# Performance work log

Hardware: AMD Instinct MI355X
Metric: run time of the kernel (lower is better)

Reference implementation:

```python
import jax, jax.numpy as jnp
import numpy as np

B, S, D, UNITS = 8, 2048, 512, 512

def setup_inputs() -> dict:
    key = jax.random.key(0)
    k1, k2, k3, k4 = jax.random.split(key, 4)
    scale = 1.0 / np.sqrt(D)
    return {
        "x": jax.random.normal(k1, (B, S, D), dtype=jnp.float32),
        "Wq": jax.random.normal(k2, (D, UNITS), dtype=jnp.float32) * scale,
        "Wk": jax.random.normal(k3, (D, UNITS), dtype=jnp.float32) * scale,
        "Wv": jax.random.normal(k4, (D, UNITS), dtype=jnp.float32) * scale,
    }

def reference(x, Wq, Wk, Wv):
    # Q, K, V: [B, S, units]
    Q = jnp.einsum('bsd,du->bsu', x, Wq)
    Km = jnp.einsum('bsd,du->bsu', x, Wk)
    V = jnp.einsum('bsd,du->bsu', x, Wv)
    d_k = jnp.asarray(Wq.shape[-1], dtype=x.dtype)
    # scores: [B, S, S]
    scores = jnp.einsum('bqu,bku->bqk', Q, Km) / jnp.sqrt(d_k)
    attn = jax.nn.softmax(scores, axis=-1)
    return jnp.einsum('bqk,bku->bqu', attn, V)
```

## Files before the change

### kernel.cpp

```cpp
#include <hip/hip_runtime.h>

typedef __attribute__((ext_vector_type(8))) __bf16 bf16x8;
typedef __attribute__((ext_vector_type(4))) float f32x4;
typedef unsigned short u16;
typedef unsigned int u32;

#define VMCNT(n) asm volatile("s_waitcnt vmcnt(" #n ")" ::: "memory")

__device__ __forceinline__ u16 f2bf(float f) {
  union { float f; u32 u; } v; v.f = f;
  u32 r = v.u + 0x7FFFu + ((v.u >> 16) & 1u);
  return (u16)(r >> 16);
}
__device__ __forceinline__ float fexp2(float x) {
  float r; asm("v_exp_f32 %0, %1" : "=v"(r) : "v"(x)); return r;
}

__global__ __launch_bounds__(256) void cast_x_kernel(const float* __restrict__ x,
                                                     u16* __restrict__ xb, int n4) {
  int i = blockIdx.x * 256 + threadIdx.x;
  if (i >= n4) return;
  float4 v = reinterpret_cast<const float4*>(x)[i];
  ushort4 o;
  o.x = f2bf(v.x); o.y = f2bf(v.y); o.z = f2bf(v.z); o.w = f2bf(v.w);
  reinterpret_cast<ushort4*>(xb)[i] = o;
}

__global__ __launch_bounds__(1024) void transpose_w_kernel(const float* __restrict__ Wq,
                                                           const float* __restrict__ Wk,
                                                           const float* __restrict__ Wv,
                                                           u16* __restrict__ Wt) {
  const float* src = blockIdx.z == 0 ? Wq : (blockIdx.z == 1 ? Wk : Wv);
  u16* dst = Wt + (size_t)blockIdx.z * 512 * 512;
  __shared__ float tile[32][33];
  int u0 = blockIdx.x * 32, d0 = blockIdx.y * 32;
  tile[threadIdx.y][threadIdx.x] = src[(d0 + threadIdx.y) * 512 + u0 + threadIdx.x];
  __syncthreads();
  dst[(u0 + threadIdx.y) * 512 + d0 + threadIdx.x] = f2bf(tile[threadIdx.x][threadIdx.y]);
}

__global__ __launch_bounds__(256) void qkv_kernel(const u16* __restrict__ Xb,
                                                  const u16* __restrict__ Wt3,
                                                  u16* __restrict__ Q, u16* __restrict__ K,
                                                  u16* __restrict__ Vt) {
  __shared__ u16 As[3][128 * 32], Bs[3][128 * 32];
  const int bm = blockIdx.y * 128;
  const int bn = blockIdx.x * 128;
  const int z = blockIdx.z;
  const u16* A = Xb + (size_t)bm * 512;
  const u16* Bt = Wt3 + (size_t)z * 512 * 512 + (size_t)bn * 512;

  const int t = threadIdx.x;
  const int lane = t & 63;
  const int w = t >> 6;
  const int wr = w >> 1, wc = w & 1;
  const int la = lane & 15;
  const int q = lane >> 4;
  f32x4 acc[4][4] = {};

  auto stage = [&](int buf, int kt) {
    const int k0 = kt * 32;
#pragma unroll
    for (int it = 0; it < 2; ++it) {
      int c = it * 256 + t, row = c >> 2;
      int col = ((c & 3) ^ ((row >> 1) & 3)) << 3;
      __builtin_amdgcn_global_load_lds(
          (const __attribute__((address_space(1))) void*)(A + (size_t)row * 512 + k0 + col),
          (__attribute__((address_space(3))) void*)(&As[buf][c * 8]), 16, 0, 0);
    }
#pragma unroll
    for (int it = 0; it < 2; ++it) {
      int c = it * 256 + t, row = c >> 2;
      int col = ((c & 3) ^ ((row >> 1) & 3)) << 3;
      __builtin_amdgcn_global_load_lds(
          (const __attribute__((address_space(1))) void*)(Bt + (size_t)row * 512 + k0 + col),
          (__attribute__((address_space(3))) void*)(&Bs[buf][c * 8]), 16, 0, 0);
    }
  };

  auto body = [&](int buf) {
    bf16x8 a[4], b[4];
#pragma unroll
    for (int i = 0; i < 4; ++i) {
      int row = wr * 64 + i * 16 + la;
      a[i] = *reinterpret_cast<const bf16x8*>(&As[buf][row * 32 + ((q ^ ((row >> 1) & 3)) << 3)]);
    }
#pragma unroll
    for (int j = 0; j < 4; ++j) {
      int row = wc * 64 + j * 16 + la;
      b[j] = *reinterpret_cast<const bf16x8*>(&Bs[buf][row * 32 + ((q ^ ((row >> 1) & 3)) << 3)]);
    }
    __builtin_amdgcn_s_setprio(1);
#pragma unroll
    for (int i = 0; i < 4; ++i)
#pragma unroll
      for (int j = 0; j < 4; ++j)
        acc[i][j] = __builtin_amdgcn_mfma_f32_16x16x32_bf16(a[i], b[j], acc[i][j], 0, 0, 0);
    __builtin_amdgcn_s_setprio(0);
  };

  stage(0, 0); stage(1, 1);
  int cb = 0, sb = 2;
  for (int kt = 0; kt < 14; ++kt) {
    VMCNT(4);
    __builtin_amdgcn_s_barrier();
    stage(sb, kt + 2);
    body(cb);
    cb = (cb == 2) ? 0 : cb + 1;
    sb = (sb == 2) ? 0 : sb + 1;
  }
  VMCNT(4); __builtin_amdgcn_s_barrier(); body(2);
  VMCNT(0); __builtin_amdgcn_s_barrier(); body(0);

  const int r0 = q * 4, cn = lane & 15;
  if (z < 2) {
    u16* out = (z == 0) ? Q : K;
#pragma unroll
    for (int i = 0; i < 4; ++i)
#pragma unroll
      for (int j = 0; j < 4; ++j)
#pragma unroll
        for (int r = 0; r < 4; ++r) {
          int m = bm + 64 * wr + 16 * i + r0 + r;
          int n = bn + 64 * wc + 16 * j + cn;
          out[(size_t)m * 512 + n] = f2bf(acc[i][j][r]);
        }
  } else {
#pragma unroll
    for (int i = 0; i < 4; ++i)
#pragma unroll
      for (int j = 0; j < 4; ++j)
#pragma unroll
        for (int r = 0; r < 4; ++r) {
          int m = bm + 64 * wr + 16 * i + r0 + r;
          int u = bn + 64 * wc + 16 * j + cn;
          int b = m >> 11, s = m & 2047;
          Vt[((size_t)b * 512 + u) * 2048 + s] = f2bf(acc[i][j][r]);
        }
  }
}

__global__ __launch_bounds__(512) void scores8_kernel(const u16* __restrict__ Q,
                                                      const u16* __restrict__ K,
                                                      u16* __restrict__ S) {
  __shared__ u16 ring[4][2][256 * 32];
  const int bb = blockIdx.x;
  const int bm = blockIdx.y * 256;
  const int bn = blockIdx.z * 256;
  const u16* Aq = Q + (size_t)(bb * 2048 + bm) * 512;
  const u16* Bk = K + (size_t)(bb * 2048 + bn) * 512;

  const int t = threadIdx.x;
  const int lane = t & 63;
  const int wid = t >> 6;
  const int wm = wid >> 2, wn = wid & 3;
  const int la = lane & 15;
  const int q = lane >> 4;

  f32x4 acc[8][4] = {};

  auto stage = [&](int kt) {
    const int r = kt & 3;
    const int koff = kt * 32;
#pragma unroll
    for (int half = 0; half < 2; ++half) {
      int c = half * 512 + t;
      int row = c >> 2;
      int col = ((c & 3) ^ ((row >> 1) & 3)) << 3;
      __builtin_amdgcn_global_load_lds(
          (const __attribute__((address_space(1))) void*)(Aq + (size_t)row * 512 + koff + col),
          (__attribute__((address_space(3))) void*)(&ring[r][0][c * 8]), 16, 0, 0);
      __builtin_amdgcn_global_load_lds(
          (const __attribute__((address_space(1))) void*)(Bk + (size_t)row * 512 + koff + col),
          (__attribute__((address_space(3))) void*)(&ring[r][1][c * 8]), 16, 0, 0);
    }
  };

  auto body = [&](int kt) {
    const int r = kt & 3;
    const u16* At = ring[r][0];
    const u16* Bt = ring[r][1];
    bf16x8 bfr[4], afr[8];
#pragma unroll
    for (int j = 0; j < 4; ++j) {
      int row = wn * 64 + j * 16 + la;
      bfr[j] = *reinterpret_cast<const bf16x8*>(Bt + row * 32 + ((q ^ ((row >> 1) & 3)) << 3));
    }
#pragma unroll
    for (int i = 0; i < 8; ++i) {
      int row = wm * 128 + i * 16 + la;
      afr[i] = *reinterpret_cast<const bf16x8*>(At + row * 32 + ((q ^ ((row >> 1) & 3)) << 3));
    }
    __builtin_amdgcn_s_setprio(1);
#pragma unroll
    for (int i = 0; i < 8; ++i)
#pragma unroll
      for (int j = 0; j < 4; ++j)
        acc[i][j] = __builtin_amdgcn_mfma_f32_16x16x32_bf16(afr[i], bfr[j], acc[i][j], 0, 0, 0);
    __builtin_amdgcn_s_setprio(0);
  };

  stage(0); stage(1); stage(2);
  for (int kt = 0; kt < 13; ++kt) {
    VMCNT(8);
    __builtin_amdgcn_s_barrier();
    stage(kt + 3);
    body(kt);
  }
  VMCNT(8); __builtin_amdgcn_s_barrier(); body(13);
  VMCNT(4); __builtin_amdgcn_s_barrier(); body(14);
  VMCNT(0); __builtin_amdgcn_s_barrier(); body(15);

  u16* C = S + (size_t)bb * 2048 * 2048;
  const float scale = 0.06375872127f;
  const int r0h = q * 4;
#pragma unroll
  for (int i = 0; i < 8; ++i)
#pragma unroll
    for (int j = 0; j < 4; ++j)
#pragma unroll
      for (int r = 0; r < 4; ++r) {
        int m = bm + wm * 128 + i * 16 + r0h + r;
        int n = bn + wn * 64 + j * 16 + la;
        C[(size_t)m * 2048 + n] = f2bf(fexp2(acc[i][j][r] * scale));
      }
}

__global__ __launch_bounds__(256) void pv_kernel(const u16* __restrict__ S,
                                                 const u16* __restrict__ Vt,
                                                 float* __restrict__ out) {
  __shared__ u16 As[4][128 * 32], Bs[4][128 * 32];
  __shared__ float larr[128];
  const int id = blockIdx.x;
  const int b = id & 7;
  const int local = id >> 3;
  const int bn = (local & 3) * 128;
  const int bm = (local >> 2) * 128;

  const u16* A = S + (size_t)(b * 2048 + bm) * 2048;
  const u16* Bt = Vt + ((size_t)b * 512 + bn) * 2048;

  const int t = threadIdx.x;
  const int lane = t & 63;
  const int w = t >> 6;
  const int wr = w >> 1, wc = w & 1;
  const int la = lane & 15;
  const int q = lane >> 4;
  f32x4 acc[4][4] = {};
  float lacc[4] = {0.f, 0.f, 0.f, 0.f};

  auto stage = [&](int kt) {
    const int buf = kt & 3;
    const int k0 = kt * 32;
#pragma unroll
    for (int it = 0; it < 2; ++it) {
      int c = it * 256 + t, row = c >> 2;
      int col = ((c & 3) ^ ((row >> 1) & 3)) << 3;
      __builtin_amdgcn_global_load_lds(
          (const __attribute__((address_space(1))) void*)(A + (size_t)row * 2048 + k0 + col),
          (__attribute__((address_space(3))) void*)(&As[buf][c * 8]), 16, 0, 0);
    }
#pragma unroll
    for (int it = 0; it < 2; ++it) {
      int c = it * 256 + t, row = c >> 2;
      int col = ((c & 3) ^ ((row >> 1) & 3)) << 3;
      __builtin_amdgcn_global_load_lds(
          (const __attribute__((address_space(1))) void*)(Bt + (size_t)row * 2048 + k0 + col),
          (__attribute__((address_space(3))) void*)(&Bs[buf][c * 8]), 16, 0, 0);
    }
  };

  auto body = [&](int kt) {
    const int buf = kt & 3;
    bf16x8 a[4], bb[4];
#pragma unroll
    for (int i = 0; i < 4; ++i) {
      int row = wr * 64 + i * 16 + la;
      a[i] = *reinterpret_cast<const bf16x8*>(&As[buf][row * 32 + ((q ^ ((row >> 1) & 3)) << 3)]);
    }
    if (wc == 0) {
#pragma unroll
      for (int i = 0; i < 4; ++i) {
        float ls = 0.f;
#pragma unroll
        for (int e = 0; e < 8; ++e) ls += (float)a[i][e];
        lacc[i] += ls;
      }
    }
#pragma unroll
    for (int j = 0; j < 4; ++j) {
      int row = wc * 64 + j * 16 + la;
      bb[j] = *reinterpret_cast<const bf16x8*>(&Bs[buf][row * 32 + ((q ^ ((row >> 1) & 3)) << 3)]);
    }
    __builtin_amdgcn_s_setprio(1);
#pragma unroll
    for (int i = 0; i < 4; ++i)
#pragma unroll
      for (int j = 0; j < 4; ++j)
        acc[i][j] = __builtin_amdgcn_mfma_f32_16x16x32_bf16(a[i], bb[j], acc[i][j], 0, 0, 0);
    __builtin_amdgcn_s_setprio(0);
  };

  stage(0); stage(1); stage(2);
  for (int kt = 0; kt < 61; ++kt) {
    VMCNT(8);
    __builtin_amdgcn_s_barrier();
    stage(kt + 3);
    body(kt);
  }
  VMCNT(8); __builtin_amdgcn_s_barrier(); body(61);
  VMCNT(4); __builtin_amdgcn_s_barrier(); body(62);
  VMCNT(0); __builtin_amdgcn_s_barrier(); body(63);

  float l[4];
#pragma unroll
  for (int i = 0; i < 4; ++i) {
    l[i] = lacc[i];
    l[i] += __shfl_xor(l[i], 16);
    l[i] += __shfl_xor(l[i], 32);
  }
  if (wc == 0 && q == 0) {
#pragma unroll
    for (int i = 0; i < 4; ++i) larr[wr * 64 + i * 16 + la] = l[i];
  }
  __syncthreads();

  float* C = out + ((size_t)b * 2048 + bm) * 512;
  const int r0 = q * 4, cn = lane & 15;
  float inv[4][4];
#pragma unroll
  for (int i = 0; i < 4; ++i)
#pragma unroll
    for (int r = 0; r < 4; ++r)
      inv[i][r] = 1.0f / larr[wr * 64 + i * 16 + r0 + r];
#pragma unroll
  for (int i = 0; i < 4; ++i)
#pragma unroll
    for (int j = 0; j < 4; ++j)
#pragma unroll
      for (int r = 0; r < 4; ++r) {
        int m = 64 * wr + 16 * i + r0 + r;
        int n = bn + 64 * wc + 16 * j + cn;
        C[(size_t)m * 512 + n] = acc[i][j][r] * inv[i][r];
      }
}

extern "C" void kernel_launch(void* const* d_in, const int* in_sizes, int n_in,
                              void* d_out, int out_size, void* d_ws, size_t ws_size,
                              hipStream_t stream) {
  const float* x  = (const float*)d_in[0];
  const float* Wq = (const float*)d_in[1];
  const float* Wk = (const float*)d_in[2];
  const float* Wv = (const float*)d_in[3];
  float* out = (float*)d_out;

  char* p = (char*)d_ws;
  u16* Xb = (u16*)p;            p += (size_t)16384 * 512 * 2;
  u16* Wt = (u16*)p;            p += (size_t)3 * 512 * 512 * 2;
  u16* Q  = (u16*)p;            p += (size_t)16384 * 512 * 2;
  u16* K  = (u16*)p;            p += (size_t)16384 * 512 * 2;
  u16* Vt = (u16*)p;            p += (size_t)16384 * 512 * 2;
  u16* S  = (u16*)p;

  cast_x_kernel<<<dim3(8192), dim3(256), 0, stream>>>(x, Xb, 16384 * 512 / 4);
  transpose_w_kernel<<<dim3(16, 16, 3), dim3(32, 32), 0, stream>>>(Wq, Wk, Wv, Wt);
  qkv_kernel<<<dim3(4, 128, 3), dim3(256), 0, stream>>>(Xb, Wt, Q, K, Vt);
  scores8_kernel<<<dim3(8, 8, 8), dim3(512), 0, stream>>>(Q, K, S);
  pv_kernel<<<dim3(512), dim3(256), 0, stream>>>(S, Vt, out);
}
```

Measured before the change: 153.8 us.

## Store scores and V in k-tiled blocked layout for contiguous PV tile loads

Changes the intermediate score matrix and transposed V to a blocked layout where each 32-wide k-slice is stored contiguously ([b][k/32][row][32]). The PV kernel's per-stage tile loads then read one contiguous 8 KB or 2 KB block instead of 128 rows strided by 4 KB, which is meant to improve DRAM/TLB locality. The scores kernel's epilogue writes become strided by 64 bytes per row, which may make its stores less coalesced.

```diff
diff --git a/kernel.cpp b/kernel.cpp
--- a/kernel.cpp
+++ b/kernel.cpp
@@ -42,7 +42,7 @@
 __global__ __launch_bounds__(256) void qkv_kernel(const u16* __restrict__ Xb,
                                                   const u16* __restrict__ Wt3,
                                                   u16* __restrict__ Q, u16* __restrict__ K,
-                                                  u16* __restrict__ Vt) {
+                                                  u16* __restrict__ Vt2) {
   __shared__ u16 As[3][128 * 32], Bs[3][128 * 32];
   const int bm = blockIdx.y * 128;
   const int bn = blockIdx.x * 128;
@@ -135,14 +135,14 @@
           int m = bm + 64 * wr + 16 * i + r0 + r;
           int u = bn + 64 * wc + 16 * j + cn;
           int b = m >> 11, s = m & 2047;
-          Vt[((size_t)b * 512 + u) * 2048 + s] = f2bf(acc[i][j][r]);
+          Vt2[(((size_t)b * 64 + (s >> 5)) * 512 + u) * 32 + (s & 31)] = f2bf(acc[i][j][r]);
         }
   }
 }
 
 __global__ __launch_bounds__(512) void scores8_kernel(const u16* __restrict__ Q,
                                                       const u16* __restrict__ K,
-                                                      u16* __restrict__ S) {
+                                                      u16* __restrict__ S2) {
   __shared__ u16 ring[4][2][256 * 32];
   const int bb = blockIdx.x;
   const int bm = blockIdx.y * 256;
@@ -211,23 +211,26 @@
   VMCNT(4); __builtin_amdgcn_s_barrier(); body(14);
   VMCNT(0); __builtin_amdgcn_s_barrier(); body(15);
 
-  u16* C = S + (size_t)bb * 2048 * 2048;
   const float scale = 0.06375872127f;
   const int r0h = q * 4;
 #pragma unroll
   for (int i = 0; i < 8; ++i)
 #pragma unroll
-    for (int j = 0; j < 4; ++j)
+    for (int j = 0; j < 4; ++j) {
+      int n = bn + wn * 64 + j * 16;
+      int kt_j = n >> 5;
+      int ke_j = (n & 31) + la;
+      u16* dst = S2 + ((size_t)(bb * 64 + kt_j) * 2048) * 32 + ke_j;
 #pragma unroll
       for (int r = 0; r < 4; ++r) {
         int m = bm + wm * 128 + i * 16 + r0h + r;
-        int n = bn + wn * 64 + j * 16 + la;
-        C[(size_t)m * 2048 + n] = f2bf(fexp2(acc[i][j][r] * scale));
+        dst[(size_t)m * 32] = f2bf(fexp2(acc[i][j][r] * scale));
       }
-}
-
-__global__ __launch_bounds__(256) void pv_kernel(const u16* __restrict__ S,
-                                                 const u16* __restrict__ Vt,
+    }
+}
+
+__global__ __launch_bounds__(256) void pv_kernel(const u16* __restrict__ S2,
+                                                 const u16* __restrict__ Vt2,
                                                  float* __restrict__ out) {
   __shared__ u16 As[4][128 * 32], Bs[4][128 * 32];
   __shared__ float larr[128];
@@ -237,8 +240,8 @@
   const int bn = (local & 3) * 128;
   const int bm = (local >> 2) * 128;
 
-  const u16* A = S + (size_t)(b * 2048 + bm) * 2048;
-  const u16* Bt = Vt + ((size_t)b * 512 + bn) * 2048;
+  const u16* A2 = S2 + ((size_t)b * 64 * 2048 + (size_t)bm) * 32;
+  const u16* B2 = Vt2 + ((size_t)b * 64 * 512 + (size_t)bn) * 32;
 
   const int t = threadIdx.x;
   const int lane = t & 63;
@@ -251,13 +254,14 @@
 
   auto stage = [&](int kt) {
     const int buf = kt & 3;
-    const int k0 = kt * 32;
+    const u16* At = A2 + (size_t)kt * 65536;
+    const u16* Bt = B2 + (size_t)kt * 16384;
 #pragma unroll
     for (int it = 0; it < 2; ++it) {
       int c = it * 256 + t, row = c >> 2;
       int col = ((c & 3) ^ ((row >> 1) & 3)) << 3;
       __builtin_amdgcn_global_load_lds(
-          (const __attribute__((address_space(1))) void*)(A + (size_t)row * 2048 + k0 + col),
+          (const __attribute__((address_space(1))) void*)(At + row * 32 + col),
           (__attribute__((address_space(3))) void*)(&As[buf][c * 8]), 16, 0, 0);
     }
 #pragma unroll
@@ -265,7 +269,7 @@
       int c = it * 256 + t, row = c >> 2;
       int col = ((c & 3) ^ ((row >> 1) & 3)) << 3;
       __builtin_amdgcn_global_load_lds(
-          (const __attribute__((address_space(1))) void*)(Bt + (size_t)row * 2048 + k0 + col),
+          (const __attribute__((address_space(1))) void*)(Bt + row * 32 + col),
           (__attribute__((address_space(3))) void*)(&Bs[buf][c * 8]), 16, 0, 0);
     }
   };
@@ -359,12 +363,12 @@
   u16* Wt = (u16*)p;            p += (size_t)3 * 512 * 512 * 2;
   u16* Q  = (u16*)p;            p += (size_t)16384 * 512 * 2;
   u16* K  = (u16*)p;            p += (size_t)16384 * 512 * 2;
-  u16* Vt = (u16*)p;            p += (size_t)16384 * 512 * 2;
-  u16* S  = (u16*)p;
+  u16* Vt2 = (u16*)p;           p += (size_t)16384 * 512 * 2;
+  u16* S2 = (u16*)p;
 
   cast_x_kernel<<<dim3(8192), dim3(256), 0, stream>>>(x, Xb, 16384 * 512 / 4);
   transpose_w_kernel<<<dim3(16, 16, 3), dim3(32, 32), 0, stream>>>(Wq, Wk, Wv, Wt);
-  qkv_kernel<<<dim3(4, 128, 3), dim3(256), 0, stream>>>(Xb, Wt, Q, K, Vt);
-  scores8_kernel<<<dim3(8, 8, 8), dim3(512), 0, stream>>>(Q, K, S);
-  pv_kernel<<<dim3(512), dim3(256), 0, stream>>>(S, Vt, out);
-}
+  qkv_kernel<<<dim3(4, 128, 3), dim3(256), 0, stream>>>(Xb, Wt, Q, K, Vt2);
+  scores8_kernel<<<dim3(8, 8, 8), dim3(512), 0, stream>>>(Q, K, S2);
+  pv_kernel<<<dim3(512), dim3(256), 0, stream>>>(S2, Vt2, out);
+}
```

Result: faster. 149.9 us (-2.5%).
